# Performance work log

Measured on AMD Instinct MI355X. Metric: run time of the kernel, lower is better.

The kernel has to match this reference:

```python
import jax, jax.numpy as jnp
import numpy as np

B, T, D = 16, 512, 384
MAX_DUR = 8          # durations drawn from [0, MAX_DUR)
OUT_LEN = T * (MAX_DUR - 1)  # static upper bound on total expanded length
PAD_VALUE = 0.0


def setup_inputs() -> dict:
    key = jax.random.key(0)
    k1, k2, k3 = jax.random.split(key, 3)
    xs = jax.random.normal(k1, (B, T, D), dtype=jnp.float32)
    ds = jax.random.randint(k2, (B, T), 0, MAX_DUR, dtype=jnp.int32)
    ilens = jax.random.randint(k3, (B,), T // 2, T + 1, dtype=jnp.int32)
    return {"xs": xs, "ds": ds, "ilens": ilens}


def reference(xs, ds, ilens):
    # Zero out durations past each sequence's valid length (equiv. to x[:ilen], d[:ilen]).
    t_src = jnp.arange(T, dtype=jnp.int32)
    d_eff = jnp.where(t_src[None, :] < ilens[:, None], ds, 0)        # (B, T)
    csum = jnp.cumsum(d_eff, axis=1)                                 # (B, T) inclusive cumsum
    total = csum[:, -1]                                              # (B,) expanded lengths

    # For each output frame t, source index i is smallest i with csum[i] > t.
    t_out = jnp.arange(OUT_LEN, dtype=jnp.int32)                     # (OUT_LEN,)
    idx = jax.vmap(lambda c: jnp.searchsorted(c, t_out, side="right"))(csum)  # (B, OUT_LEN)
    idx = jnp.minimum(idx, T - 1)

    out = jnp.take_along_axis(xs, idx[:, :, None], axis=1)           # (B, OUT_LEN, D)
    valid = t_out[None, :] < total[:, None]                          # (B, OUT_LEN)
    return jnp.where(valid[:, :, None], out, jnp.asarray(PAD_VALUE, xs.dtype))
```

## Files before the change

### kernel.cpp

```cpp
#include <hip/hip_runtime.h>

#define B_SZ 16
#define T_SZ 512
#define D_SZ 384
#define MAX_DUR 8
#define OUT_LEN (T_SZ * (MAX_DUR - 1))
#define D4 (D_SZ / 4)
#define TOTAL4 (B_SZ * OUT_LEN * D4)

__global__ void __launch_bounds__(T_SZ) scan_search_kernel(
    const int* __restrict__ ds,
    const int* __restrict__ ilens,
    int* __restrict__ idx_out)
{
    __shared__ int s[T_SZ];
    const int b = blockIdx.x;
    const int t = threadIdx.x;
    const int ilen = ilens[b];

    int val = (t < ilen) ? ds[b * T_SZ + t] : 0;
    s[t] = val;
    __syncthreads();

    #pragma unroll
    for (int off = 1; off < T_SZ; off <<= 1) {
        int add = (t >= off) ? s[t - off] : 0;
        __syncthreads();
        s[t] += add;
        __syncthreads();
    }

    const int total = s[T_SZ - 1];

    for (int k = t; k < OUT_LEN; k += T_SZ) {
        int lo = 0, hi = T_SZ;
        while (lo < hi) {
            int mid = (lo + hi) >> 1;
            if (s[mid] <= k) lo = mid + 1; else hi = mid;
        }
        int idx = lo < (T_SZ - 1) ? lo : (T_SZ - 1);
        idx_out[b * OUT_LEN + k] = (k < total) ? idx : -1;
    }
}

__global__ void __launch_bounds__(256) gather_kernel(
    const float4* __restrict__ xs,
    const int* __restrict__ idx,
    float4* __restrict__ out)
{
    int gid = blockIdx.x * 256 + threadIdx.x;
    if (gid >= TOTAL4) return;

    int row = gid / D4;
    int d4  = gid - row * D4;
    int i   = idx[row];

    float4 v;
    if (i < 0) {
        v.x = 0.f; v.y = 0.f; v.z = 0.f; v.w = 0.f;
    } else {
        int b = row / OUT_LEN;
        v = xs[(b * T_SZ + i) * D4 + d4];
    }
    out[gid] = v;
}

extern "C" void kernel_launch(void* const* d_in, const int* in_sizes, int n_in,
                              void* d_out, int out_size, void* d_ws, size_t ws_size,
                              hipStream_t stream) {
    const float* xs    = (const float*)d_in[0];
    const int*   ds    = (const int*)d_in[1];
    const int*   ilens = (const int*)d_in[2];
    float*       out   = (float*)d_out;
    int*         idx   = (int*)d_ws;

    scan_search_kernel<<<B_SZ, T_SZ, 0, stream>>>(ds, ilens, idx);

    constexpr int nblk = (TOTAL4 + 255) / 256;
    gather_kernel<<<nblk, 256, 0, stream>>>(
        (const float4*)xs, idx, (float4*)out);
}
```

Baseline: 109.6 us.

## Fuse duration scan, search and gather into one tiled kernel

Merges the scan/search kernel and the gather kernel into a single launch. Each block recomputes the per-batch cumulative sum with a wave-shuffle scan, binary-searches source indices for a 64-row output tile into shared memory, then copies the rows. This removes a second launch and the global index round trip. In exchange the scan is repeated redundantly in all 56 tile blocks of each batch.

```diff
diff --git a/kernel.cpp b/kernel.cpp
--- a/kernel.cpp
+++ b/kernel.cpp
@@ -5,64 +5,76 @@
 #define D_SZ 384
 #define MAX_DUR 8
 #define OUT_LEN (T_SZ * (MAX_DUR - 1))
-#define D4 (D_SZ / 4)
-#define TOTAL4 (B_SZ * OUT_LEN * D4)
+#define D4 96
+#define TILE 64
+#define NTILE (OUT_LEN / TILE)
+#define NTHREADS 256
 
-__global__ void __launch_bounds__(T_SZ) scan_search_kernel(
-    const int* __restrict__ ds,
-    const int* __restrict__ ilens,
-    int* __restrict__ idx_out)
+__global__ void __launch_bounds__(NTHREADS) lenreg_fused_kernel(
+    const float4* __restrict__ xs,
+    const int*    __restrict__ ds,
+    const int*    __restrict__ ilens,
+    float4*       __restrict__ out)
 {
-    __shared__ int s[T_SZ];
-    const int b = blockIdx.x;
-    const int t = threadIdx.x;
+    __shared__ int s_csum[T_SZ];
+    __shared__ int s_wave[4];
+    __shared__ int s_idx[TILE];
+
+    const int t    = threadIdx.x;
+    const int tile = blockIdx.x;
+    const int b    = blockIdx.y;
+    const int lane = t & 63;
+    const int w    = t >> 6;
+
     const int ilen = ilens[b];
 
-    int val = (t < ilen) ? ds[b * T_SZ + t] : 0;
-    s[t] = val;
+    const int2 dv = ((const int2*)(ds + b * T_SZ))[t];
+    const int i0 = 2 * t, i1 = 2 * t + 1;
+    int v0 = (i0 < ilen) ? dv.x : 0;
+    int v1 = (i1 < ilen) ? dv.y : 0;
+
+    int x = v0 + v1;
+    #pragma unroll
+    for (int off = 1; off < 64; off <<= 1) {
+        int y = __shfl_up(x, off, 64);
+        if (lane >= off) x += y;
+    }
+    if (lane == 63) s_wave[w] = x;
+    __syncthreads();
+    int base = 0;
+    #pragma unroll
+    for (int i = 0; i < 3; ++i)
+        if (i < w) base += s_wave[i];
+    const int c1 = base + x;
+    s_csum[i1] = c1;
+    s_csum[i0] = c1 - v1;
     __syncthreads();
 
-    #pragma unroll
-    for (int off = 1; off < T_SZ; off <<= 1) {
-        int add = (t >= off) ? s[t - off] : 0;
-        __syncthreads();
-        s[t] += add;
-        __syncthreads();
-    }
+    const int total = s_csum[T_SZ - 1];
 
-    const int total = s[T_SZ - 1];
-
-    for (int k = t; k < OUT_LEN; k += T_SZ) {
+    if (t < TILE) {
+        const int k = tile * TILE + t;
         int lo = 0, hi = T_SZ;
         while (lo < hi) {
             int mid = (lo + hi) >> 1;
-            if (s[mid] <= k) lo = mid + 1; else hi = mid;
+            if (s_csum[mid] <= k) lo = mid + 1; else hi = mid;
         }
         int idx = lo < (T_SZ - 1) ? lo : (T_SZ - 1);
-        idx_out[b * OUT_LEN + k] = (k < total) ? idx : -1;
+        s_idx[t] = (k < total) ? idx : -1;
     }
-}
+    __syncthreads();
 
-__global__ void __launch_bounds__(256) gather_kernel(
-    const float4* __restrict__ xs,
-    const int* __restrict__ idx,
-    float4* __restrict__ out)
-{
-    int gid = blockIdx.x * 256 + threadIdx.x;
-    if (gid >= TOTAL4) return;
-
-    int row = gid / D4;
-    int d4  = gid - row * D4;
-    int i   = idx[row];
-
-    float4 v;
-    if (i < 0) {
-        v.x = 0.f; v.y = 0.f; v.z = 0.f; v.w = 0.f;
-    } else {
-        int b = row / OUT_LEN;
-        v = xs[(b * T_SZ + i) * D4 + d4];
+    const float4* xsrow  = xs  + (size_t)b * T_SZ * D4;
+    float4*       outrow = out + ((size_t)b * OUT_LEN + (size_t)tile * TILE) * D4;
+    #pragma unroll
+    for (int j = t; j < TILE * D4; j += NTHREADS) {
+        const int r  = j / D4;
+        const int d4 = j - r * D4;
+        const int i  = s_idx[r];
+        float4 v = {0.f, 0.f, 0.f, 0.f};
+        if (i >= 0) v = xsrow[i * D4 + d4];
+        outrow[j] = v;
     }
-    out[gid] = v;
 }
 
 extern "C" void kernel_launch(void* const* d_in, const int* in_sizes, int n_in,
@@ -72,11 +84,8 @@
     const int*   ds    = (const int*)d_in[1];
     const int*   ilens = (const int*)d_in[2];
     float*       out   = (float*)d_out;
-    int*         idx   = (int*)d_ws;
 
-    scan_search_kernel<<<B_SZ, T_SZ, 0, stream>>>(ds, ilens, idx);
-
-    constexpr int nblk = (TOTAL4 + 255) / 256;
-    gather_kernel<<<nblk, 256, 0, stream>>>(
-        (const float4*)xs, idx, (float4*)out);
+    dim3 grid(NTILE, B_SZ);
+    lenreg_fused_kernel<<<grid, NTHREADS, 0, stream>>>(
+        (const float4*)xs, ds, ilens, (float4*)out);
 }
```

Result: no change. 111.5 us (+1.7%).
